# Performance work log

Measured on AMD Instinct MI355X. Metric: run time of the kernel, lower is better.

The kernel has to match this reference:

```python
import jax, jax.numpy as jnp
import numpy as np

GROUP_SIZE = 128

def setup_inputs() -> dict:
    key = jax.random.key(0)
    k1, k2, k3, k4 = jax.random.split(key, 4)
    in_f, out_f = 4096, 4096
    num_groups = (in_f + GROUP_SIZE - 1) // GROUP_SIZE  # 32
    x = jax.random.normal(k1, (4, 2048, in_f), dtype=jnp.float32)
    qweight = jax.random.randint(k2, (out_f, in_f), 0, 16, dtype=jnp.int32)
    scales = jax.random.uniform(k3, (out_f, num_groups), dtype=jnp.float32)
    bias = jax.random.normal(k4, (out_f,), dtype=jnp.float32)
    return {"x": x, "qweight": qweight, "scales": scales, "bias": bias}

def reference(x, qweight, scales, bias):
    out_f, in_f = qweight.shape
    # group-wise dequantize: broadcast each per-group scale over its columns
    scale_full = jnp.repeat(scales, GROUP_SIZE, axis=1)[:, :in_f]  # [out, in]
    weight = qweight.astype(scales.dtype) * scale_full             # [out, in]
    # F.linear(x, weight, bias) == x @ weight.T + bias
    return jnp.einsum('bsi,oi->bso', x, weight) + bias
```

## Files before the change

kernel.cpp:

```cpp
#include <hip/hip_runtime.h>
#include <hip/hip_bf16.h>

typedef __bf16 bf16_t;
typedef __bf16 bf16x8 __attribute__((ext_vector_type(8)));
typedef float  f32x4  __attribute__((ext_vector_type(4)));

static constexpr int M_ = 8192;
static constexpr int N_ = 4096;
static constexpr int K_ = 4096;
static constexpr int BM = 128, BN = 128, BK = 32;

__device__ __forceinline__ void load_lds16(const bf16_t* g, bf16_t* l) {
  __builtin_amdgcn_global_load_lds(
      (const __attribute__((address_space(1))) void*)g,
      (__attribute__((address_space(3))) void*)l,
      16, 0, 0);
}

__global__ __launch_bounds__(256) void cvt_x_kernel(const float* __restrict__ x,
                                                    bf16_t* __restrict__ xb) {
  const size_t i = ((size_t)blockIdx.x * 256 + threadIdx.x) * 8;
  const float4 f0 = *(const float4*)(x + i);
  const float4 f1 = *(const float4*)(x + i + 4);
  bf16x8 o;
  o[0] = (bf16_t)f0.x; o[1] = (bf16_t)f0.y; o[2] = (bf16_t)f0.z; o[3] = (bf16_t)f0.w;
  o[4] = (bf16_t)f1.x; o[5] = (bf16_t)f1.y; o[6] = (bf16_t)f1.z; o[7] = (bf16_t)f1.w;
  *(bf16x8*)(xb + i) = o;
}

__global__ __launch_bounds__(256) void dequant_kernel(const int* __restrict__ q,
                                                      const float* __restrict__ s,
                                                      bf16_t* __restrict__ wb) {
  const size_t base = ((size_t)blockIdx.x * 256 + threadIdx.x) * 8;
  const int o  = (int)(base >> 12);
  const int ii = (int)(base & 4095);
  const float sc = s[(o << 5) + (ii >> 7)];
  const int4 q0 = *(const int4*)(q + base);
  const int4 q1 = *(const int4*)(q + base + 4);
  bf16x8 w;
  w[0] = (bf16_t)((float)q0.x * sc); w[1] = (bf16_t)((float)q0.y * sc);
  w[2] = (bf16_t)((float)q0.z * sc); w[3] = (bf16_t)((float)q0.w * sc);
  w[4] = (bf16_t)((float)q1.x * sc); w[5] = (bf16_t)((float)q1.y * sc);
  w[6] = (bf16_t)((float)q1.z * sc); w[7] = (bf16_t)((float)q1.w * sc);
  *(bf16x8*)(wb + base) = w;
}

__global__ __launch_bounds__(256) void gemm_kernel(const bf16_t* __restrict__ A,
                                                   const bf16_t* __restrict__ B,
                                                   const float* __restrict__ bias,
                                                   float* __restrict__ C) {
  __shared__ __align__(16) bf16_t As[BM * BK];
  __shared__ __align__(16) bf16_t Bs[BN * BK];

  const int tid  = threadIdx.x;
  const int lane = tid & 63;
  const int wave = tid >> 6;
  const int bm = blockIdx.y * BM;
  const int bn = blockIdx.x * BN;
  const int wm = (wave & 1) * 64;
  const int wn = (wave >> 1) * 64;
  const int ln = lane & 15;
  const int lq = lane >> 4;

  const int r0 = tid >> 2;
  const int c0 = (tid & 3) * 8;
  const bf16_t* a0 = A + (size_t)(bm + r0) * K_ + c0;
  const bf16_t* a1 = A + (size_t)(bm + r0 + 64) * K_ + c0;
  const bf16_t* b0 = B + (size_t)(bn + r0) * K_ + c0;
  const bf16_t* b1 = B + (size_t)(bn + r0 + 64) * K_ + c0;
  bf16_t* lA0 = As + (size_t)tid * 8;
  bf16_t* lA1 = As + (size_t)(tid + 256) * 8;
  bf16_t* lB0 = Bs + (size_t)tid * 8;
  bf16_t* lB1 = Bs + (size_t)(tid + 256) * 8;

  f32x4 acc[4][4] = {};

  for (int kt = 0; kt < K_; kt += BK) {
    load_lds16(a0 + kt, lA0);
    load_lds16(a1 + kt, lA1);
    load_lds16(b0 + kt, lB0);
    load_lds16(b1 + kt, lB1);
    __syncthreads();

    bf16x8 af[4], bq[4];
#pragma unroll
    for (int i = 0; i < 4; ++i)
      af[i] = *(const bf16x8*)(As + (wm + i * 16 + ln) * BK + lq * 8);
#pragma unroll
    for (int j = 0; j < 4; ++j)
      bq[j] = *(const bf16x8*)(Bs + (wn + j * 16 + ln) * BK + lq * 8);
#pragma unroll
    for (int i = 0; i < 4; ++i)
#pragma unroll
      for (int j = 0; j < 4; ++j)
        acc[i][j] = __builtin_amdgcn_mfma_f32_16x16x32_bf16(af[i], bq[j], acc[i][j], 0, 0, 0);

    __syncthreads();
  }

#pragma unroll
  for (int j = 0; j < 4; ++j) {
    const int col = bn + wn + j * 16 + ln;
    const float bv = bias[col];
#pragma unroll
    for (int i = 0; i < 4; ++i) {
      const int row0 = bm + wm + i * 16 + lq * 4;
      float* cp = C + (size_t)row0 * N_ + col;
#pragma unroll
      for (int r = 0; r < 4; ++r) {
        *cp = acc[i][j][r] + bv;
        cp += N_;
      }
    }
  }
}

extern "C" void kernel_launch(void* const* d_in, const int* in_sizes, int n_in,
                              void* d_out, int out_size, void* d_ws, size_t ws_size,
                              hipStream_t stream) {
  const float* x    = (const float*)d_in[0];
  const int*   qw   = (const int*)d_in[1];
  const float* sc   = (const float*)d_in[2];
  const float* bias = (const float*)d_in[3];
  float* out = (float*)d_out;

  bf16_t* xb = (bf16_t*)d_ws;
  bf16_t* wb = xb + (size_t)M_ * K_;

  cvt_x_kernel<<<(int)(((size_t)M_ * K_) / (256 * 8)), 256, 0, stream>>>(x, xb);
  dequant_kernel<<<(int)(((size_t)N_ * K_) / (256 * 8)), 256, 0, stream>>>(qw, sc, wb);

  dim3 grid(N_ / BN, M_ / BM);
  gemm_kernel<<<grid, 256, 0, stream>>>(xb, wb, bias, out);
}
```

Measured before the change: 572.1 us.

## Use 256x256x64 tiles with double-buffered LDS, XOR swizzle, and XCD-aware block mapping

Reworks the GEMM to use 256x256 output tiles with BK=64, 512 threads (8 waves, each computing 128x64), and double-buffered LDS, so the next K tile loads while the current one is computed. It adds an XOR swizzle on LDS columns to avoid bank conflicts, remaps the 1D grid so neighbouring tiles land on the same XCD for L2 reuse, and brackets the MFMA groups with setprio. The goal is more data reuse per load and hiding global latency. The cost is higher register pressure from 32 accumulators per thread, 128KB of LDS, and launch_bounds(512,2) occupancy that may not be achievable.

```diff
diff --git a/kernel.cpp b/kernel.cpp
--- a/kernel.cpp
+++ b/kernel.cpp
@@ -8,7 +8,10 @@
 static constexpr int M_ = 8192;
 static constexpr int N_ = 4096;
 static constexpr int K_ = 4096;
-static constexpr int BM = 128, BN = 128, BK = 32;
+
+static constexpr int BM = 256, BN = 256, BK = 64;
+static constexpr int NT = K_ / BK;
+static constexpr int LDS_TILE = BM * BK;
 
 __device__ __forceinline__ void load_lds16(const bf16_t* g, bf16_t* l) {
   __builtin_amdgcn_global_load_lds(
@@ -45,66 +48,137 @@
   *(bf16x8*)(wb + base) = w;
 }
 
-__global__ __launch_bounds__(256) void gemm_kernel(const bf16_t* __restrict__ A,
-                                                   const bf16_t* __restrict__ B,
-                                                   const float* __restrict__ bias,
-                                                   float* __restrict__ C) {
-  __shared__ __align__(16) bf16_t As[BM * BK];
-  __shared__ __align__(16) bf16_t Bs[BN * BK];
+__global__ __launch_bounds__(512, 2) void gemm_kernel(const bf16_t* __restrict__ A,
+                                                      const bf16_t* __restrict__ B,
+                                                      const float* __restrict__ bias,
+                                                      float* __restrict__ C) {
+  __shared__ __align__(16) bf16_t As[2][LDS_TILE];
+  __shared__ __align__(16) bf16_t Bs[2][LDS_TILE];
 
   const int tid  = threadIdx.x;
   const int lane = tid & 63;
   const int wave = tid >> 6;
-  const int bm = blockIdx.y * BM;
-  const int bn = blockIdx.x * BN;
-  const int wm = (wave & 1) * 64;
-  const int wn = (wave >> 1) * 64;
   const int ln = lane & 15;
   const int lq = lane >> 4;
-
-  const int r0 = tid >> 2;
-  const int c0 = (tid & 3) * 8;
-  const bf16_t* a0 = A + (size_t)(bm + r0) * K_ + c0;
-  const bf16_t* a1 = A + (size_t)(bm + r0 + 64) * K_ + c0;
-  const bf16_t* b0 = B + (size_t)(bn + r0) * K_ + c0;
-  const bf16_t* b1 = B + (size_t)(bn + r0 + 64) * K_ + c0;
-  bf16_t* lA0 = As + (size_t)tid * 8;
-  bf16_t* lA1 = As + (size_t)(tid + 256) * 8;
-  bf16_t* lB0 = Bs + (size_t)tid * 8;
-  bf16_t* lB1 = Bs + (size_t)(tid + 256) * 8;
-
-  f32x4 acc[4][4] = {};
-
-  for (int kt = 0; kt < K_; kt += BK) {
-    load_lds16(a0 + kt, lA0);
-    load_lds16(a1 + kt, lA1);
-    load_lds16(b0 + kt, lB0);
-    load_lds16(b1 + kt, lB1);
-    __syncthreads();
-
-    bf16x8 af[4], bq[4];
-#pragma unroll
-    for (int i = 0; i < 4; ++i)
-      af[i] = *(const bf16x8*)(As + (wm + i * 16 + ln) * BK + lq * 8);
-#pragma unroll
-    for (int j = 0; j < 4; ++j)
-      bq[j] = *(const bf16x8*)(Bs + (wn + j * 16 + ln) * BK + lq * 8);
-#pragma unroll
-    for (int i = 0; i < 4; ++i)
-#pragma unroll
-      for (int j = 0; j < 4; ++j)
-        acc[i][j] = __builtin_amdgcn_mfma_f32_16x16x32_bf16(af[i], bq[j], acc[i][j], 0, 0, 0);
-
-    __syncthreads();
+  const int wm = wave >> 2;
+  const int wn = wave & 3;
+
+  const int bid = blockIdx.x;
+  const int wg  = (bid & 7) * 64 + (bid >> 3);
+  const int bn  = (wg & 15) * BN;
+  const int bm  = (wg >> 4) * BM;
+
+  const int r_sub = tid >> 3;
+  const int g_col = (((tid & 7) ^ (r_sub & 7)) * 8);
+  const size_t a_off = (size_t)(bm + r_sub) * K_ + g_col;
+  const size_t b_off = (size_t)(bn + r_sub) * K_ + g_col;
+  const int lds_off = tid * 8;
+
+  const int kx0 = (lq * 8) ^ ((ln & 7) * 8);
+  const int kx1 = (32 + lq * 8) ^ ((ln & 7) * 8);
+  const int a_rb = (wm * 128 + ln) * BK;
+  const int b_rb = (wn * 64 + ln) * BK;
+
+  f32x4 acc[8][4] = {};
+
+#pragma unroll
+  for (int c = 0; c < 4; ++c)
+    load_lds16(A + a_off + (size_t)c * 64 * K_, &As[0][c * 4096 + lds_off]);
+#pragma unroll
+  for (int c = 0; c < 4; ++c)
+    load_lds16(B + b_off + (size_t)c * 64 * K_, &Bs[0][c * 4096 + lds_off]);
+
+  for (int t = 0; t < NT; ++t) {
+    const int buf = t & 1;
+    if (t + 1 < NT) {
+      const size_t kt1 = (size_t)(t + 1) * BK;
+#pragma unroll
+      for (int c = 0; c < 4; ++c)
+        load_lds16(A + a_off + kt1 + (size_t)c * 64 * K_, &As[buf ^ 1][c * 4096 + lds_off]);
+#pragma unroll
+      for (int c = 0; c < 4; ++c)
+        load_lds16(B + b_off + kt1 + (size_t)c * 64 * K_, &Bs[buf ^ 1][c * 4096 + lds_off]);
+      asm volatile("s_waitcnt vmcnt(8)" ::: "memory");
+    } else {
+      asm volatile("s_waitcnt vmcnt(0)" ::: "memory");
+    }
+    __builtin_amdgcn_s_barrier();
+    __builtin_amdgcn_sched_barrier(0);
+
+    const bf16_t* as = As[buf];
+    const bf16_t* bs = Bs[buf];
+    bf16x8 af[4][2], bq[4][2];
+
+#pragma unroll
+    for (int i = 0; i < 4; ++i) {
+      af[i][0] = *(const bf16x8*)(as + a_rb + i * 16 * BK + kx0);
+      af[i][1] = *(const bf16x8*)(as + a_rb + i * 16 * BK + kx1);
+    }
+#pragma unroll
+    for (int j = 0; j < 2; ++j) {
+      bq[j][0] = *(const bf16x8*)(bs + b_rb + j * 16 * BK + kx0);
+      bq[j][1] = *(const bf16x8*)(bs + b_rb + j * 16 * BK + kx1);
+    }
+    __builtin_amdgcn_s_setprio(1);
+#pragma unroll
+    for (int i = 0; i < 4; ++i)
+#pragma unroll
+      for (int j = 0; j < 2; ++j) {
+        acc[i][j] = __builtin_amdgcn_mfma_f32_16x16x32_bf16(af[i][0], bq[j][0], acc[i][j], 0, 0, 0);
+        acc[i][j] = __builtin_amdgcn_mfma_f32_16x16x32_bf16(af[i][1], bq[j][1], acc[i][j], 0, 0, 0);
+      }
+    __builtin_amdgcn_s_setprio(0);
+
+#pragma unroll
+    for (int j = 2; j < 4; ++j) {
+      bq[j][0] = *(const bf16x8*)(bs + b_rb + j * 16 * BK + kx0);
+      bq[j][1] = *(const bf16x8*)(bs + b_rb + j * 16 * BK + kx1);
+    }
+    __builtin_amdgcn_s_setprio(1);
+#pragma unroll
+    for (int i = 0; i < 4; ++i)
+#pragma unroll
+      for (int j = 2; j < 4; ++j) {
+        acc[i][j] = __builtin_amdgcn_mfma_f32_16x16x32_bf16(af[i][0], bq[j][0], acc[i][j], 0, 0, 0);
+        acc[i][j] = __builtin_amdgcn_mfma_f32_16x16x32_bf16(af[i][1], bq[j][1], acc[i][j], 0, 0, 0);
+      }
+    __builtin_amdgcn_s_setprio(0);
+
+#pragma unroll
+    for (int i = 0; i < 4; ++i) {
+      af[i][0] = *(const bf16x8*)(as + a_rb + (i + 4) * 16 * BK + kx0);
+      af[i][1] = *(const bf16x8*)(as + a_rb + (i + 4) * 16 * BK + kx1);
+    }
+    __builtin_amdgcn_s_setprio(1);
+#pragma unroll
+    for (int i = 0; i < 4; ++i)
+#pragma unroll
+      for (int j = 2; j < 4; ++j) {
+        acc[i + 4][j] = __builtin_amdgcn_mfma_f32_16x16x32_bf16(af[i][0], bq[j][0], acc[i + 4][j], 0, 0, 0);
+        acc[i + 4][j] = __builtin_amdgcn_mfma_f32_16x16x32_bf16(af[i][1], bq[j][1], acc[i + 4][j], 0, 0, 0);
+      }
+    __builtin_amdgcn_s_setprio(0);
+
+    __builtin_amdgcn_s_setprio(1);
+#pragma unroll
+    for (int i = 0; i < 4; ++i)
+#pragma unroll
+      for (int j = 0; j < 2; ++j) {
+        acc[i + 4][j] = __builtin_amdgcn_mfma_f32_16x16x32_bf16(af[i][0], bq[j][0], acc[i + 4][j], 0, 0, 0);
+        acc[i + 4][j] = __builtin_amdgcn_mfma_f32_16x16x32_bf16(af[i][1], bq[j][1], acc[i + 4][j], 0, 0, 0);
+      }
+    __builtin_amdgcn_s_setprio(0);
+
+    __builtin_amdgcn_s_barrier();
   }
 
 #pragma unroll
   for (int j = 0; j < 4; ++j) {
-    const int col = bn + wn + j * 16 + ln;
+    const int col = bn + wn * 64 + j * 16 + ln;
     const float bv = bias[col];
 #pragma unroll
-    for (int i = 0; i < 4; ++i) {
-      const int row0 = bm + wm + i * 16 + lq * 4;
+    for (int i = 0; i < 8; ++i) {
+      const int row0 = bm + wm * 128 + i * 16 + lq * 4;
       float* cp = C + (size_t)row0 * N_ + col;
 #pragma unroll
       for (int r = 0; r < 4; ++r) {
@@ -130,6 +204,6 @@
   cvt_x_kernel<<<(int)(((size_t)M_ * K_) / (256 * 8)), 256, 0, stream>>>(x, xb);
   dequant_kernel<<<(int)(((size_t)N_ * K_) / (256 * 8)), 256, 0, stream>>>(qw, sc, wb);
 
-  dim3 grid(N_ / BN, M_ / BM);
-  gemm_kernel<<<grid, 256, 0, stream>>>(xb, wb, bias, out);
-}
+  const int nwg = (N_ / BN) * (M_ / BM);
+  gemm_kernel<<<nwg, 512, 0, stream>>>(xb, wb, bias, out);
+}
```

Result: faster. 551.5 us (-3.6%).
